# Performance work log

Measured on AMD Instinct MI355X. Metric: run time of the kernel, lower is better.

Reference implementation:

```python
import jax, jax.numpy as jnp
import numpy as np

B, T, C = 4, 4096, 256

def setup_inputs() -> dict:
    key = jax.random.key(0)
    kx, km, kk, kq, kv = jax.random.split(key, 5)
    x = jax.random.normal(kx, (B, T, C), dtype=jnp.float32)
    mask = jax.random.randint(km, (B, T), 0, 2, dtype=jnp.int32)
    s = C ** -0.5
    Wk = jax.random.normal(kk, (C, C), dtype=jnp.float32) * s
    Wq = jax.random.normal(kq, (C, C), dtype=jnp.float32) * s
    Wv = jax.random.normal(kv, (C, C), dtype=jnp.float32) * s
    return {"x": x, "mask": mask, "Wk": Wk, "Wq": Wq, "Wv": Wv}

def reference(x, mask, Wk, Wq, Wv):
    # nn.Linear: y = x @ W.T  (W is [out, in])
    k = jnp.einsum('btc,dc->btd', x, Wk)   # [B,T,C]
    q = jnp.einsum('btc,dc->btd', x, Wq)   # [B,T,C]
    v = jnp.einsum('btc,dc->btd', x, Wv)   # [B,T,C]
    scale = k.shape[-1] ** -0.5
    weights = jnp.einsum('bqc,bkc->bqk', q, k) * scale  # [B,T,T]
    # torch quirk: mask.float().masked_fill(mask==0, -inf) adds +1.0 where mask!=0
    mask_f = jnp.where(mask == 0, -jnp.inf, mask.astype(weights.dtype))  # [B,T]
    masked = weights + mask_f[:, None, :]   # broadcast over query dim == repeat(1,T,1)
    attn = jax.nn.softmax(masked, axis=-1)
    out = jnp.einsum('bqk,bkc->bqc', attn, v)  # [B,T,C]
    return out
```

## Files before the change

kernel.cpp:

```cpp
#include <hip/hip_runtime.h>


typedef __attribute__((ext_vector_type(8)))  _Float16 f16x8;
typedef __attribute__((ext_vector_type(4)))  _Float16 f16x4;
typedef __attribute__((ext_vector_type(4)))  float    f32x4;
typedef __attribute__((ext_vector_type(16))) float    f32x16;

constexpr int Bb = 4;
constexpr int Tt = 4096;
constexpr int Cc = 256;
constexpr int BT = Bb * Tt;
constexpr int NT = 64;

#define MFMA16(a, b, c) __builtin_amdgcn_mfma_f32_16x16x32_f16((a), (b), (c), 0, 0, 0)
#define MFMA32(a, b, c) __builtin_amdgcn_mfma_f32_32x32x16_f16((a), (b), (c), 0, 0, 0)

__device__ __forceinline__ void gl16(const _Float16* gp, char* lp) {
    __builtin_amdgcn_global_load_lds(
        (const __attribute__((address_space(1))) void*)gp,
        (__attribute__((address_space(3))) void*)lp, 16, 0, 0);
}

__global__ __launch_bounds__(256) void qkv_proj(
    const float* __restrict__ x,
    const float* __restrict__ Wq, const float* __restrict__ Wk,
    const float* __restrict__ Wv,
    _Float16* __restrict__ qo, _Float16* __restrict__ ko,
    _Float16* __restrict__ vto)
{
    extern __shared__ _Float16 sm[];
    _Float16* xs = sm;
    _Float16* wsm = sm + 128 * 264;

    const int tid = threadIdx.x;
    const int m0  = blockIdx.x * 128;
    const int ny  = blockIdx.y;
    const int mat = ny >> 1;
    const int d0  = (ny & 1) * 128;
    const float* W = (mat == 0) ? Wq : (mat == 1 ? Wk : Wv);

#pragma unroll
    for (int i = 0; i < 32; ++i) {
        int flat = i * 256 + tid;
        int r = flat >> 6, c4 = (flat & 63) << 2;
        float4 v = *reinterpret_cast<const float4*>(x + (size_t)(m0 + r) * Cc + c4);
        f16x4 h = { (_Float16)v.x, (_Float16)v.y, (_Float16)v.z, (_Float16)v.w };
        *reinterpret_cast<f16x4*>(xs + r * 264 + c4) = h;
    }
#pragma unroll
    for (int i = 0; i < 32; ++i) {
        int flat = i * 256 + tid;
        int r = flat >> 6, c4 = (flat & 63) << 2;
        float4 v = *reinterpret_cast<const float4*>(W + (size_t)(d0 + r) * Cc + c4);
        f16x4 h = { (_Float16)v.x, (_Float16)v.y, (_Float16)v.z, (_Float16)v.w };
        *reinterpret_cast<f16x4*>(wsm + r * 264 + c4) = h;
    }
    __syncthreads();

    const int w = tid >> 6, lane = tid & 63;
    const int lr = lane & 15, lg = lane >> 4;

    f32x4 acc[2][8] = {};

#pragma unroll
    for (int kc = 0; kc < 8; ++kc) {
        const int c0 = kc * 32 + lg * 8;
        f16x8 xf[2], wf[8];
#pragma unroll
        for (int mb = 0; mb < 2; ++mb)
            xf[mb] = *reinterpret_cast<const f16x8*>(xs + (w * 32 + mb * 16 + lr) * 264 + c0);
#pragma unroll
        for (int db = 0; db < 8; ++db)
            wf[db] = *reinterpret_cast<const f16x8*>(wsm + (db * 16 + lr) * 264 + c0);
        if (mat != 2) {
#pragma unroll
            for (int mb = 0; mb < 2; ++mb)
#pragma unroll
                for (int db = 0; db < 8; ++db)
                    acc[mb][db] = MFMA16(wf[db], xf[mb], acc[mb][db]);
        } else {
#pragma unroll
            for (int mb = 0; mb < 2; ++mb)
#pragma unroll
                for (int db = 0; db < 8; ++db)
                    acc[mb][db] = MFMA16(xf[mb], wf[db], acc[mb][db]);
        }
    }

    if (mat != 2) {
        const float sc = (mat == 0) ? 0.0625f * 1.44269504f : 1.0f;
        const int jj  = (lg & 1) * 4;
#pragma unroll
        for (int mb = 0; mb < 2; ++mb)
#pragma unroll
            for (int db = 0; db < 8; ++db) {
                int m  = m0 + w * 32 + mb * 16 + lr;
                int c  = d0 + db * 16 + lg * 4;
                int kc = c >> 5;
                int ch = (c >> 3) & 3;
                f32x4 a = acc[mb][db];
                f16x4 h = { (_Float16)(a.x * sc), (_Float16)(a.y * sc),
                            (_Float16)(a.z * sc), (_Float16)(a.w * sc) };
                if (mat == 0) {
                    size_t off = (size_t)(m >> 5) * 8192 + (((m >> 4) & 1) * 8 + kc) * 512
                               + ch * 128 + (m & 15) * 8 + jj;
                    *reinterpret_cast<f16x4*>(qo + off) = h;
                } else {
                    size_t off = (size_t)(m >> 4) * 4096 + kc * 512
                               + ch * 128 + (m & 15) * 8 + jj;
                    *reinterpret_cast<f16x4*>(ko + off) = h;
                }
            }
    } else {
        const int jj = (lg & 1) * 4;
        const int kh = (lg >> 1) & 1;
#pragma unroll
        for (int mb = 0; mb < 2; ++mb)
#pragma unroll
            for (int db = 0; db < 8; ++db) {
                int d = d0 + db * 16 + lr;
                int m = m0 + w * 32 + mb * 16 + lg * 4;
                f32x4 a = acc[mb][db];
                f16x4 h = { (_Float16)a.x, (_Float16)a.y, (_Float16)a.z, (_Float16)a.w };
                size_t off = (size_t)(m >> 4) * 4096 + (d >> 5) * 512
                           + kh * 256 + (d & 31) * 8 + jj;
                *reinterpret_cast<f16x4*>(vto + off) = h;
            }
    }
}

__global__ __launch_bounds__(512, 2) void attn_kernel(
    const _Float16* __restrict__ qb, const _Float16* __restrict__ kb,
    const _Float16* __restrict__ vtb, const int* __restrict__ mask,
    float* __restrict__ outp)
{
    extern __shared__ char smraw[];
    float* mex32 = (float*)(smraw + 151552);
    float* lex32 = (float*)(smraw + 152576);
    float* oexf  = (float*)smraw;

    const int tid = threadIdx.x, w = tid >> 6, lane = tid & 63;
    const int qw = w >> 2, g = w & 3;
    const int l15 = lane & 15, l4 = lane >> 4;
    const int l31 = lane & 31, l5 = lane >> 5;

    const int bid = blockIdx.x;
    const int b   = (bid & 7) >> 1;
    const int qt  = ((bid >> 3) << 1) | (bid & 1);
    const int q0  = qt * 64;
    const size_t base = (size_t)b * Tt * Cc;
    const int* maskb = mask + (size_t)b * Tt;
    const _Float16* kTb = kb + base;
    const _Float16* vTb = vtb + base;

    f16x8 qf[2][8];
    {
        const _Float16* qTb = qb + (size_t)(b * 128 + qt * 2 + qw) * 8192;
#pragma unroll
        for (int qh = 0; qh < 2; ++qh)
#pragma unroll
            for (int kc = 0; kc < 8; ++kc)
                qf[qh][kc] = *reinterpret_cast<const f16x8*>(
                    qTb + (qh * 8 + kc) * 512 + l4 * 128 + l15 * 8);
    }

    char* kreg = smraw + g * 16384;
    char* vreg = smraw + 65536 + g * 16384;
    _Float16* pw = (_Float16*)(smraw + 131072) + w * 1280;

    f32x16 o[8] = {};
    float m0r = -60.f, m1r = -60.f, l0r = 0.f, l1r = 0.f;

    auto STAGE_K = [&](int t) {
        char* dst = kreg + (t & 1) * 8192;
        const _Float16* src = kTb + (size_t)(t * 4 + g) * 4096 + lane * 8;
#pragma unroll
        for (int j = 0; j < 8; ++j) gl16(src + j * 512, dst + j * 1024);
    };
    auto STAGE_V = [&](int t) {
        char* dst = vreg + (t & 1) * 8192;
        const _Float16* src = vTb + (size_t)(t * 4 + g) * 4096 + lane * 8;
#pragma unroll
        for (int j = 0; j < 8; ++j) gl16(src + j * 512, dst + j * 1024);
    };

    if (qw == 0) STAGE_K(0);
    asm volatile("s_waitcnt vmcnt(0)" ::: "memory");

    f32x4 s00, s01, s10, s11;

#pragma unroll 1
    for (int t = 0; t < NT; ++t) {
        __syncthreads();
        if (qw == 0) { if (t + 1 < NT) STAGE_K(t + 1); }
        else if (!(t & 1)) { STAGE_V(t); if (t + 1 < NT) STAGE_V(t + 1); }

        const _Float16* kb_ = (const _Float16*)(kreg + (t & 1) * 8192);
        int4 mc = *reinterpret_cast<const int4*>(maskb + (t * 4 + g) * 16 + l4 * 4);

        f32x4 sa = { 0.f, 0.f, 0.f, 0.f }, sb = { 0.f, 0.f, 0.f, 0.f };
        __builtin_amdgcn_s_setprio(1);
#pragma unroll
        for (int kc = 0; kc < 8; ++kc) {
            f16x8 kf = *reinterpret_cast<const f16x8*>(kb_ + kc * 512 + l4 * 128 + l15 * 8);
            sa = MFMA16(kf, qf[0][kc], sa);
            sb = MFMA16(kf, qf[1][kc], sb);
        }
        __builtin_amdgcn_s_setprio(0);

        if (mc.x == 0) { sa[0] = -1e30f; sb[0] = -1e30f; }
        if (mc.y == 0) { sa[1] = -1e30f; sb[1] = -1e30f; }
        if (mc.z == 0) { sa[2] = -1e30f; sb[2] = -1e30f; }
        if (mc.w == 0) { sa[3] = -1e30f; sb[3] = -1e30f; }

        if (!(t & 1)) {
            s00 = sa; s01 = sb;
        } else {
            s10 = sa; s11 = sb;

            float t0 = fmaxf(fmaxf(fmaxf(s00[0], s00[1]), fmaxf(s00[2], s00[3])),
                             fmaxf(fmaxf(s10[0], s10[1]), fmaxf(s10[2], s10[3])));
            float t1 = fmaxf(fmaxf(fmaxf(s01[0], s01[1]), fmaxf(s01[2], s01[3])),
                             fmaxf(fmaxf(s11[0], s11[1]), fmaxf(s11[2], s11[3])));
            t0 = fmaxf(t0, __shfl_xor(t0, 16, 64)); t0 = fmaxf(t0, __shfl_xor(t0, 32, 64));
            t1 = fmaxf(t1, __shfl_xor(t1, 16, 64)); t1 = fmaxf(t1, __shfl_xor(t1, 32, 64));

            if (__any(t0 > m0r + 11.54f || t1 > m1r + 11.54f)) {
                float mn0 = fmaxf(m0r, t0), mn1 = fmaxf(m1r, t1);
                float c0 = exp2f(m0r - mn0), c1 = exp2f(m1r - mn1);
                m0r = mn0; m1r = mn1; l0r *= c0; l1r *= c1;
                float cs = (lane & 16) ? c1 : c0;
#pragma unroll
                for (int dt = 0; dt < 8; ++dt) o[dt] *= cs;
            }

            float rs0 = 0.f, rs1 = 0.f;
#pragma unroll
            for (int r = 0; r < 4; ++r) {
                float p;
                p = exp2f(s00[r] - m0r); s00[r] = p; rs0 += p;
                p = exp2f(s10[r] - m0r); s10[r] = p; rs0 += p;
                p = exp2f(s01[r] - m1r); s01[r] = p; rs1 += p;
                p = exp2f(s11[r] - m1r); s11[r] = p; rs1 += p;
            }
            rs0 += __shfl_xor(rs0, 16, 64); rs0 += __shfl_xor(rs0, 32, 64);
            rs1 += __shfl_xor(rs1, 16, 64); rs1 += __shfl_xor(rs1, 32, 64);
            l0r += rs0; l1r += rs1;

            {
                f16x4 h;
                h = (f16x4){ (_Float16)s00[0], (_Float16)s00[1], (_Float16)s00[2], (_Float16)s00[3] };
                *reinterpret_cast<f16x4*>(pw + l15 * 40 + l4 * 4) = h;
                h = (f16x4){ (_Float16)s10[0], (_Float16)s10[1], (_Float16)s10[2], (_Float16)s10[3] };
                *reinterpret_cast<f16x4*>(pw + l15 * 40 + 16 + l4 * 4) = h;
                h = (f16x4){ (_Float16)s01[0], (_Float16)s01[1], (_Float16)s01[2], (_Float16)s01[3] };
                *reinterpret_cast<f16x4*>(pw + (16 + l15) * 40 + l4 * 4) = h;
                h = (f16x4){ (_Float16)s11[0], (_Float16)s11[1], (_Float16)s11[2], (_Float16)s11[3] };
                *reinterpret_cast<f16x4*>(pw + (16 + l15) * 40 + 16 + l4 * 4) = h;
            }
            f16x8 pf0 = *reinterpret_cast<const f16x8*>(pw + l31 * 40 + l5 * 8);
            f16x8 pf1 = *reinterpret_cast<const f16x8*>(pw + l31 * 40 + 16 + l5 * 8);

            __builtin_amdgcn_s_setprio(1);
#pragma unroll
            for (int dt = 0; dt < 8; ++dt) {
                f16x8 vf0 = *reinterpret_cast<const f16x8*>(
                    vreg + 0 * 8192 + dt * 1024 + l5 * 512 + l31 * 16);
                o[dt] = MFMA32(vf0, pf0, o[dt]);
                f16x8 vf1 = *reinterpret_cast<const f16x8*>(
                    vreg + 1 * 8192 + dt * 1024 + l5 * 512 + l31 * 16);
                o[dt] = MFMA32(vf1, pf1, o[dt]);
            }
            __builtin_amdgcn_s_setprio(0);
        }

        asm volatile("s_waitcnt vmcnt(0)" ::: "memory");
    }
    __syncthreads();

    if (l4 == 0) {
        mex32[(qw * 4 + g) * 32 + l15]      = m0r;
        mex32[(qw * 4 + g) * 32 + 16 + l15] = m1r;
        lex32[(qw * 4 + g) * 32 + l15]      = l0r;
        lex32[(qw * 4 + g) * 32 + 16 + l15] = l1r;
    }
    __syncthreads();

    float mq = (lane & 16) ? m1r : m0r;
    float mst = -1e30f;
#pragma unroll
    for (int g2 = 0; g2 < 4; ++g2)
        mst = fmaxf(mst, mex32[(qw * 4 + g2) * 32 + l31]);
    float osc = exp2f(mq - mst);

#pragma unroll 1
    for (int s = 0; s < 2; ++s) {
        if (qw == s) {
            float* og = oexf + g * (32 * 258);
#pragma unroll
            for (int dt = 0; dt < 8; ++dt)
#pragma unroll
                for (int r = 0; r < 16; ++r) {
                    int d = dt * 32 + (r & 3) + 8 * (r >> 2) + 4 * l5;
                    og[l31 * 258 + d] = o[dt][r] * osc;
                }
        }
        __syncthreads();
        {
            const int q = tid >> 4, dg = tid & 15;
            float mA = mex32[(s * 4 + 0) * 32 + q], mB = mex32[(s * 4 + 1) * 32 + q];
            float mC = mex32[(s * 4 + 2) * 32 + q], mD = mex32[(s * 4 + 3) * 32 + q];
            float ms = fmaxf(fmaxf(mA, mB), fmaxf(mC, mD));
            float lt = lex32[(s * 4 + 0) * 32 + q] * exp2f(mA - ms)
                     + lex32[(s * 4 + 1) * 32 + q] * exp2f(mB - ms)
                     + lex32[(s * 4 + 2) * 32 + q] * exp2f(mC - ms)
                     + lex32[(s * 4 + 3) * 32 + q] * exp2f(mD - ms);
            float inv = 1.f / lt;
#pragma unroll
            for (int i = 0; i < 4; ++i) {
                int d0 = dg * 16 + i * 4;
                f32x4 a = *reinterpret_cast<const f32x4*>(oexf + q * 258 + d0);
#pragma unroll
                for (int g2 = 1; g2 < 4; ++g2) {
                    f32x4 tt = *reinterpret_cast<const f32x4*>(
                        oexf + g2 * (32 * 258) + q * 258 + d0);
                    a[0] += tt[0]; a[1] += tt[1]; a[2] += tt[2]; a[3] += tt[3];
                }
                a[0] *= inv; a[1] *= inv; a[2] *= inv; a[3] *= inv;
                *reinterpret_cast<f32x4*>(
                    outp + base + (size_t)(q0 + s * 32 + q) * Cc + d0) = a;
            }
        }
        __syncthreads();
    }
}

extern "C" void kernel_launch(void* const* d_in, const int* in_sizes, int n_in,
                              void* d_out, int out_size, void* d_ws, size_t ws_size,
                              hipStream_t stream)
{
    (void)in_sizes; (void)n_in; (void)out_size; (void)ws_size;
    const float* x   = (const float*)d_in[0];
    const int*  mask = (const int*)d_in[1];
    const float* Wk  = (const float*)d_in[2];
    const float* Wq  = (const float*)d_in[3];
    const float* Wv  = (const float*)d_in[4];
    float* out = (float*)d_out;

    _Float16* q  = (_Float16*)d_ws;
    _Float16* k  = q + (size_t)BT * Cc;
    _Float16* vt = k + (size_t)BT * Cc;

    dim3 gA(128, 6), blkA(256);
    size_t ldsA = (size_t)(128 + 128) * 264 * sizeof(_Float16);
    qkv_proj<<<gA, blkA, ldsA, stream>>>(x, Wq, Wk, Wv, q, k, vt);

    dim3 gB(256), blkB(512);
    size_t ldsB = 153600;
    attn_kernel<<<gB, blkB, ldsB, stream>>>(q, k, vt, mask, out);
}
```

Before: 145.6 us.

## Load K tiles directly into registers and split KV range contiguously per wave group

Result: slower. 354.0 us (+143.0%).

```diff
diff --git a/kernel.cpp b/kernel.cpp
--- a/kernel.cpp
+++ b/kernel.cpp
@@ -10,7 +10,7 @@
 constexpr int Tt = 4096;
 constexpr int Cc = 256;
 constexpr int BT = Bb * Tt;
-constexpr int NT = 64;
+constexpr int NT2 = 32;
 
 #define MFMA16(a, b, c) __builtin_amdgcn_mfma_f32_16x16x32_f16((a), (b), (c), 0, 0, 0)
 #define MFMA32(a, b, c) __builtin_amdgcn_mfma_f32_32x32x16_f16((a), (b), (c), 0, 0, 0)
@@ -129,7 +129,7 @@
     }
 }
 
-__global__ __launch_bounds__(512, 2) void attn_kernel(
+__global__ __launch_bounds__(512, 1) void attn_kernel(
     const _Float16* __restrict__ qb, const _Float16* __restrict__ kb,
     const _Float16* __restrict__ vtb, const int* __restrict__ mask,
     float* __restrict__ outp)
@@ -164,117 +164,122 @@
                     qTb + (qh * 8 + kc) * 512 + l4 * 128 + l15 * 8);
     }
 
-    char* kreg = smraw + g * 16384;
-    char* vreg = smraw + 65536 + g * 16384;
     _Float16* pw = (_Float16*)(smraw + 131072) + w * 1280;
 
     f32x16 o[8] = {};
     float m0r = -60.f, m1r = -60.f, l0r = 0.f, l1r = 0.f;
 
-    auto STAGE_K = [&](int t) {
-        char* dst = kreg + (t & 1) * 8192;
-        const _Float16* src = kTb + (size_t)(t * 4 + g) * 4096 + lane * 8;
+    f16x8 ka[8], kb2[8];
+    auto LOADK = [&](f16x8 (&kr)[8], int tile) {
+        const _Float16* src = kTb + (size_t)tile * 4096 + l4 * 128 + l15 * 8;
+#pragma unroll
+        for (int kc = 0; kc < 8; ++kc)
+            kr[kc] = *reinterpret_cast<const f16x8*>(src + kc * 512);
+    };
+    auto STAGE_V = [&](int t) {
+        char* dst = smraw + g * 32768 + (t & 1) * 16384 + qw * 8192;
+        const _Float16* src = vTb + (size_t)(g * 64 + 2 * t + qw) * 4096 + lane * 8;
 #pragma unroll
         for (int j = 0; j < 8; ++j) gl16(src + j * 512, dst + j * 1024);
     };
-    auto STAGE_V = [&](int t) {
-        char* dst = vreg + (t & 1) * 8192;
-        const _Float16* src = vTb + (size_t)(t * 4 + g) * 4096 + lane * 8;
-#pragma unroll
-        for (int j = 0; j < 8; ++j) gl16(src + j * 512, dst + j * 1024);
-    };
-
-    if (qw == 0) STAGE_K(0);
-    asm volatile("s_waitcnt vmcnt(0)" ::: "memory");
-
-    f32x4 s00, s01, s10, s11;
+
+    STAGE_V(0);
+    LOADK(ka,  g * 64 + 0);
+    LOADK(kb2, g * 64 + 1);
+    int4 mc0 = *reinterpret_cast<const int4*>(maskb + g * 1024 + l4 * 4);
+    int4 mc1 = *reinterpret_cast<const int4*>(maskb + g * 1024 + 16 + l4 * 4);
 
 #pragma unroll 1
-    for (int t = 0; t < NT; ++t) {
+    for (int t = 0; t < NT2; ++t) {
         __syncthreads();
-        if (qw == 0) { if (t + 1 < NT) STAGE_K(t + 1); }
-        else if (!(t & 1)) { STAGE_V(t); if (t + 1 < NT) STAGE_V(t + 1); }
-
-        const _Float16* kb_ = (const _Float16*)(kreg + (t & 1) * 8192);
-        int4 mc = *reinterpret_cast<const int4*>(maskb + (t * 4 + g) * 16 + l4 * 4);
-
-        f32x4 sa = { 0.f, 0.f, 0.f, 0.f }, sb = { 0.f, 0.f, 0.f, 0.f };
+        if (t + 1 < NT2) STAGE_V(t + 1);
+
+        f32x4 s00 = { 0.f, 0.f, 0.f, 0.f }, s01 = { 0.f, 0.f, 0.f, 0.f };
         __builtin_amdgcn_s_setprio(1);
 #pragma unroll
         for (int kc = 0; kc < 8; ++kc) {
-            f16x8 kf = *reinterpret_cast<const f16x8*>(kb_ + kc * 512 + l4 * 128 + l15 * 8);
-            sa = MFMA16(kf, qf[0][kc], sa);
-            sb = MFMA16(kf, qf[1][kc], sb);
+            s00 = MFMA16(ka[kc], qf[0][kc], s00);
+            s01 = MFMA16(ka[kc], qf[1][kc], s01);
         }
         __builtin_amdgcn_s_setprio(0);
-
-        if (mc.x == 0) { sa[0] = -1e30f; sb[0] = -1e30f; }
-        if (mc.y == 0) { sa[1] = -1e30f; sb[1] = -1e30f; }
-        if (mc.z == 0) { sa[2] = -1e30f; sb[2] = -1e30f; }
-        if (mc.w == 0) { sa[3] = -1e30f; sb[3] = -1e30f; }
-
-        if (!(t & 1)) {
-            s00 = sa; s01 = sb;
-        } else {
-            s10 = sa; s11 = sb;
-
-            float t0 = fmaxf(fmaxf(fmaxf(s00[0], s00[1]), fmaxf(s00[2], s00[3])),
-                             fmaxf(fmaxf(s10[0], s10[1]), fmaxf(s10[2], s10[3])));
-            float t1 = fmaxf(fmaxf(fmaxf(s01[0], s01[1]), fmaxf(s01[2], s01[3])),
-                             fmaxf(fmaxf(s11[0], s11[1]), fmaxf(s11[2], s11[3])));
-            t0 = fmaxf(t0, __shfl_xor(t0, 16, 64)); t0 = fmaxf(t0, __shfl_xor(t0, 32, 64));
-            t1 = fmaxf(t1, __shfl_xor(t1, 16, 64)); t1 = fmaxf(t1, __shfl_xor(t1, 32, 64));
-
-            if (__any(t0 > m0r + 11.54f || t1 > m1r + 11.54f)) {
-                float mn0 = fmaxf(m0r, t0), mn1 = fmaxf(m1r, t1);
-                float c0 = exp2f(m0r - mn0), c1 = exp2f(m1r - mn1);
-                m0r = mn0; m1r = mn1; l0r *= c0; l1r *= c1;
-                float cs = (lane & 16) ? c1 : c0;
-#pragma unroll
-                for (int dt = 0; dt < 8; ++dt) o[dt] *= cs;
-            }
-
-            float rs0 = 0.f, rs1 = 0.f;
-#pragma unroll
-            for (int r = 0; r < 4; ++r) {
-                float p;
-                p = exp2f(s00[r] - m0r); s00[r] = p; rs0 += p;
-                p = exp2f(s10[r] - m0r); s10[r] = p; rs0 += p;
-                p = exp2f(s01[r] - m1r); s01[r] = p; rs1 += p;
-                p = exp2f(s11[r] - m1r); s11[r] = p; rs1 += p;
-            }
-            rs0 += __shfl_xor(rs0, 16, 64); rs0 += __shfl_xor(rs0, 32, 64);
-            rs1 += __shfl_xor(rs1, 16, 64); rs1 += __shfl_xor(rs1, 32, 64);
-            l0r += rs0; l1r += rs1;
-
-            {
-                f16x4 h;
-                h = (f16x4){ (_Float16)s00[0], (_Float16)s00[1], (_Float16)s00[2], (_Float16)s00[3] };
-                *reinterpret_cast<f16x4*>(pw + l15 * 40 + l4 * 4) = h;
-                h = (f16x4){ (_Float16)s10[0], (_Float16)s10[1], (_Float16)s10[2], (_Float16)s10[3] };
-                *reinterpret_cast<f16x4*>(pw + l15 * 40 + 16 + l4 * 4) = h;
-                h = (f16x4){ (_Float16)s01[0], (_Float16)s01[1], (_Float16)s01[2], (_Float16)s01[3] };
-                *reinterpret_cast<f16x4*>(pw + (16 + l15) * 40 + l4 * 4) = h;
-                h = (f16x4){ (_Float16)s11[0], (_Float16)s11[1], (_Float16)s11[2], (_Float16)s11[3] };
-                *reinterpret_cast<f16x4*>(pw + (16 + l15) * 40 + 16 + l4 * 4) = h;
-            }
-            f16x8 pf0 = *reinterpret_cast<const f16x8*>(pw + l31 * 40 + l5 * 8);
-            f16x8 pf1 = *reinterpret_cast<const f16x8*>(pw + l31 * 40 + 16 + l5 * 8);
-
-            __builtin_amdgcn_s_setprio(1);
-#pragma unroll
-            for (int dt = 0; dt < 8; ++dt) {
-                f16x8 vf0 = *reinterpret_cast<const f16x8*>(
-                    vreg + 0 * 8192 + dt * 1024 + l5 * 512 + l31 * 16);
-                o[dt] = MFMA32(vf0, pf0, o[dt]);
-                f16x8 vf1 = *reinterpret_cast<const f16x8*>(
-                    vreg + 1 * 8192 + dt * 1024 + l5 * 512 + l31 * 16);
-                o[dt] = MFMA32(vf1, pf1, o[dt]);
-            }
-            __builtin_amdgcn_s_setprio(0);
-        }
-
-        asm volatile("s_waitcnt vmcnt(0)" ::: "memory");
+        if (t + 1 < NT2) LOADK(ka, g * 64 + 2 * (t + 1));
+
+        f32x4 s10 = { 0.f, 0.f, 0.f, 0.f }, s11 = { 0.f, 0.f, 0.f, 0.f };
+        __builtin_amdgcn_s_setprio(1);
+#pragma unroll
+        for (int kc = 0; kc < 8; ++kc) {
+            s10 = MFMA16(kb2[kc], qf[0][kc], s10);
+            s11 = MFMA16(kb2[kc], qf[1][kc], s11);
+        }
+        __builtin_amdgcn_s_setprio(0);
+        if (t + 1 < NT2) LOADK(kb2, g * 64 + 2 * (t + 1) + 1);
+
+        if (mc0.x == 0) { s00[0] = -1e30f; s01[0] = -1e30f; }
+        if (mc0.y == 0) { s00[1] = -1e30f; s01[1] = -1e30f; }
+        if (mc0.z == 0) { s00[2] = -1e30f; s01[2] = -1e30f; }
+        if (mc0.w == 0) { s00[3] = -1e30f; s01[3] = -1e30f; }
+        if (mc1.x == 0) { s10[0] = -1e30f; s11[0] = -1e30f; }
+        if (mc1.y == 0) { s10[1] = -1e30f; s11[1] = -1e30f; }
+        if (mc1.z == 0) { s10[2] = -1e30f; s11[2] = -1e30f; }
+        if (mc1.w == 0) { s10[3] = -1e30f; s11[3] = -1e30f; }
+        if (t + 1 < NT2) {
+            mc0 = *reinterpret_cast<const int4*>(maskb + g * 1024 + (t + 1) * 32 + l4 * 4);
+            mc1 = *reinterpret_cast<const int4*>(maskb + g * 1024 + (t + 1) * 32 + 16 + l4 * 4);
+        }
+
+        float t0 = fmaxf(fmaxf(fmaxf(s00[0], s00[1]), fmaxf(s00[2], s00[3])),
+                         fmaxf(fmaxf(s10[0], s10[1]), fmaxf(s10[2], s10[3])));
+        float t1 = fmaxf(fmaxf(fmaxf(s01[0], s01[1]), fmaxf(s01[2], s01[3])),
+                         fmaxf(fmaxf(s11[0], s11[1]), fmaxf(s11[2], s11[3])));
+        t0 = fmaxf(t0, __shfl_xor(t0, 16, 64)); t0 = fmaxf(t0, __shfl_xor(t0, 32, 64));
+        t1 = fmaxf(t1, __shfl_xor(t1, 16, 64)); t1 = fmaxf(t1, __shfl_xor(t1, 32, 64));
+
+        if (__any(t0 > m0r + 11.54f || t1 > m1r + 11.54f)) {
+            float mn0 = fmaxf(m0r, t0), mn1 = fmaxf(m1r, t1);
+            float c0 = exp2f(m0r - mn0), c1 = exp2f(m1r - mn1);
+            m0r = mn0; m1r = mn1; l0r *= c0; l1r *= c1;
+            float cs = (lane & 16) ? c1 : c0;
+#pragma unroll
+            for (int dt = 0; dt < 8; ++dt) o[dt] *= cs;
+        }
+
+        float rs0 = 0.f, rs1 = 0.f;
+#pragma unroll
+        for (int r = 0; r < 4; ++r) {
+            float p;
+            p = exp2f(s00[r] - m0r); s00[r] = p; rs0 += p;
+            p = exp2f(s10[r] - m0r); s10[r] = p; rs0 += p;
+            p = exp2f(s01[r] - m1r); s01[r] = p; rs1 += p;
+            p = exp2f(s11[r] - m1r); s11[r] = p; rs1 += p;
+        }
+        rs0 += __shfl_xor(rs0, 16, 64); rs0 += __shfl_xor(rs0, 32, 64);
+        rs1 += __shfl_xor(rs1, 16, 64); rs1 += __shfl_xor(rs1, 32, 64);
+        l0r += rs0; l1r += rs1;
+
+        {
+            f16x4 h;
+            h = (f16x4){ (_Float16)s00[0], (_Float16)s00[1], (_Float16)s00[2], (_Float16)s00[3] };
+            *reinterpret_cast<f16x4*>(pw + l15 * 40 + l4 * 4) = h;
+            h = (f16x4){ (_Float16)s10[0], (_Float16)s10[1], (_Float16)s10[2], (_Float16)s10[3] };
+            *reinterpret_cast<f16x4*>(pw + l15 * 40 + 16 + l4 * 4) = h;
+            h = (f16x4){ (_Float16)s01[0], (_Float16)s01[1], (_Float16)s01[2], (_Float16)s01[3] };
+            *reinterpret_cast<f16x4*>(pw + (16 + l15) * 40 + l4 * 4) = h;
+            h = (f16x4){ (_Float16)s11[0], (_Float16)s11[1], (_Float16)s11[2], (_Float16)s11[3] };
+            *reinterpret_cast<f16x4*>(pw + (16 + l15) * 40 + 16 + l4 * 4) = h;
+        }
+        f16x8 pf0 = *reinterpret_cast<const f16x8*>(pw + l31 * 40 + l5 * 8);
+        f16x8 pf1 = *reinterpret_cast<const f16x8*>(pw + l31 * 40 + 16 + l5 * 8);
+
+        const char* vb_ = smraw + g * 32768 + (t & 1) * 16384;
+        __builtin_amdgcn_s_setprio(1);
+#pragma unroll
+        for (int dt = 0; dt < 8; ++dt) {
+            f16x8 vf0 = *reinterpret_cast<const f16x8*>(vb_ + dt * 1024 + l5 * 512 + l31 * 16);
+            o[dt] = MFMA32(vf0, pf0, o[dt]);
+            f16x8 vf1 = *reinterpret_cast<const f16x8*>(vb_ + 8192 + dt * 1024 + l5 * 512 + l31 * 16);
+            o[dt] = MFMA32(vf1, pf1, o[dt]);
+        }
+        __builtin_amdgcn_s_setprio(0);
     }
     __syncthreads();
 
```
